# Performance work log

Measured on AMD Instinct MI355X. Metric: run time of the kernel, lower is better.

## Reference

```python
import jax, jax.numpy as jnp
import numpy as np

CAPS_N, DIMS_N, ROUNDS = 10, 16, 3
IN_CAPS_N, IN_DIMS_N = 1152, 8
BATCH = 256
EPS = 1e-7  # keras backend.epsilon()


def squash(x, axis=-1):
    sq = jnp.sum(x * x, axis=axis, keepdims=True)
    return (sq / (1.0 + sq)) * x / jnp.sqrt(sq + EPS)


def setup_inputs() -> dict:
    key = jax.random.key(0)
    k1, k2 = jax.random.split(key)
    inputs = jax.random.normal(k1, (BATCH, IN_CAPS_N, IN_DIMS_N), dtype=jnp.float32)
    # glorot-ish scale for the transform weights
    W = jax.random.normal(k2, (CAPS_N, IN_CAPS_N, DIMS_N, IN_DIMS_N), dtype=jnp.float32) * 0.05
    return {"inputs": inputs, "W": W}


def reference(inputs, W):
    # u_hat[b,j,i,d] = W[j,i] @ inputs[b,i]  (per-pair prediction vectors)
    u_hat = jnp.einsum('jide,bie->bjid', W, inputs)  # [B, caps_n, in_caps_n, dims_n]
    B = inputs.shape[0]
    cc = jnp.zeros((B, CAPS_N, IN_CAPS_N), dtype=u_hat.dtype)  # routing logits
    v = None
    for r in range(ROUNDS):
        c = jax.nn.softmax(cc, axis=1)                    # softmax over output capsules
        s = jnp.einsum('bji,bjid->bjd', c, u_hat)         # weighted sum over input caps
        v = squash(s, axis=-1)                            # [B, caps_n, dims_n]
        if r != ROUNDS - 1:
            cc = cc + jnp.einsum('bjid,bjd->bji', u_hat, v)  # agreement
    return v
```

## Files before the change

kernel.cpp:

```cpp
#include <hip/hip_runtime.h>

#define B_N 256
#define IC_N 1152
#define J_N 10
#define D_N 16

typedef __attribute__((ext_vector_type(8))) short short8;
typedef __attribute__((ext_vector_type(4))) float floatx4;

union u4s8 { uint4 u; short8 s; };

__device__ __forceinline__ float bf_lo(unsigned int u){
  union { unsigned int i; float f; } c; c.i = u << 16; return c.f;
}
__device__ __forceinline__ float bf_hi(unsigned int u){
  union { unsigned int i; float f; } c; c.i = u & 0xffff0000u; return c.f;
}
__device__ __forceinline__ unsigned int rne16(float f){
  union { float ff; unsigned int i; } c; c.ff = f;
  return (c.i + 0x7FFFu + ((c.i >> 16) & 1u)) >> 16;
}
__device__ __forceinline__ unsigned int pack_rne(float lo, float hi){
  return rne16(lo) | (rne16(hi) << 16);
}
__device__ __forceinline__ unsigned int pack_trunc(float lo, float hi){
  union { float f; unsigned int u; } a, b; a.f = lo; b.f = hi;
  return __builtin_amdgcn_perm(b.u, a.u, 0x07060302u);
}

__global__ __launch_bounds__(256) void caps_prep(
    const float* __restrict__ W, uint4* __restrict__ wsf,
    uint4* __restrict__ wcc2, float* __restrict__ vsum)
{
  const int tid = threadIdx.x;
  const int t0 = blockIdx.x * 256 + tid;
  if (t0 < B_N * J_N * D_N) vsum[t0] = 0.f;
  __shared__ unsigned int lw[1024];
  const int j = blockIdx.x / 72, itile = blockIdx.x % 72;
  const float4* Wt = (const float4*)(W + ((size_t)(j * IC_N + itile * 16) << 7));
  #pragma unroll
  for (int h = 0; h < 2; ++h) {
    const float4 f = Wt[h * 256 + tid];
    lw[(h * 256 + tid) * 2]     = pack_rne(f.x, f.y);
    lw[(h * 256 + tid) * 2 + 1] = pack_rne(f.z, f.w);
  }
  __syncthreads();
  {
    const int ktl = tid >> 6, ln = tid & 63;
    const int base = (ktl * 4 + (ln >> 4)) * 64 + (ln & 15) * 4;
    uint4 q;
    q.x = lw[base]; q.y = lw[base + 1]; q.z = lw[base + 2]; q.w = lw[base + 3];
    wsf[((size_t)j * 288 + itile * 4 + ktl) * 64 + ln] = q;
  }
  {
    const int e = tid >> 5, lane2 = tid & 31;
    const int il = lane2 & 15, dbase = (lane2 >> 4) * 8;
    unsigned short h[8];
    #pragma unroll
    for (int k = 0; k < 8; ++k) {
      const unsigned int u = lw[il * 64 + (dbase + k) * 4 + (e >> 1)];
      h[k] = (e & 1) ? (unsigned short)(u >> 16) : (unsigned short)(u & 0xffffu);
    }
    uint4 q;
    q.x = h[0] | ((unsigned int)h[1] << 16);
    q.y = h[2] | ((unsigned int)h[3] << 16);
    q.z = h[4] | ((unsigned int)h[5] << 16);
    q.w = h[6] | ((unsigned int)h[7] << 16);
    wcc2[(((size_t)j * 8 + e) * 72 + itile) * 32 + lane2] = q;
  }
}

__global__ __launch_bounds__(640, 5) void caps_pass(
    const float* __restrict__ x,
    const uint4* __restrict__ wsf, const uint4* __restrict__ wcc2,
    const uint4* __restrict__ vsbf, float* __restrict__ s_part, const int round)
{
  __shared__ float ccl[10 * 32 * 17];
  __shared__ unsigned int xt[32 * 17 * 4];

  const int tid  = threadIdx.x;
  const int wave = tid >> 6;
  const int lane = tid & 63;
  const int quad = lane >> 4;
  const int col  = lane & 15;

  const int bid = blockIdx.x;
  const int wid = (bid & 7) * 72 + (bid >> 3);
  const int bx  = wid & 15;
  const int by  = wid >> 4;
  const int b0  = bx << 4;
  const int i0  = by << 5;

  if (tid < 512) {
    const int b = tid >> 5, j4 = tid & 31;
    const int half = j4 & 1;
    #pragma unroll
    for (int ii = 0; ii < 2; ++ii) {
      const int i = ii * 16 + (j4 >> 1);
      const float4 v = ((const float4*)(x + ((size_t)((b0 + b) * IC_N + i0 + i) << 3)))[half];
      const int idx = ((i * 17 + b) << 2) + (half << 1);
      xt[idx]     = pack_rne(v.x, v.y);
      xt[idx + 1] = pack_rne(v.z, v.w);
    }
  }

  uint4 wf8[8];
  if (round == 0) {
    #pragma unroll
    for (int kt = 0; kt < 8; ++kt)
      wf8[kt] = wsf[((size_t)wave * 288 + (by << 3) + kt) * 64 + lane];
  }
  __syncthreads();
  const uint4* xtq = (const uint4*)xt;

  if (round > 0) {
    short8 av = {0,0,0,0,0,0,0,0};
    if (quad < 2)
      av = *(const short8*)&vsbf[((size_t)(b0 + col) * J_N + wave) * 2 + quad];
    #pragma unroll
    for (int c = 0; c < 2; ++c) {
      uint4 bvq[8];
      #pragma unroll
      for (int e = 0; e < 8; ++e) {
        uint4 q = {0u, 0u, 0u, 0u};
        if (lane < 32)
          q = wcc2[(((size_t)wave * 8 + e) * 72 + (by * 2 + c)) * 32 + lane];
        bvq[e] = q;
      }
      uint4 xr[4];
      #pragma unroll
      for (int r = 0; r < 4; ++r)
        xr[r] = xtq[(c * 16 + col) * 17 + quad * 4 + r];
      floatx4 cc4 = {0.f, 0.f, 0.f, 0.f};
      #pragma unroll
      for (int e = 0; e < 8; ++e) {
        u4s8 bv; bv.u = bvq[e];
        floatx4 tf = {0.f, 0.f, 0.f, 0.f};
        tf = __builtin_amdgcn_mfma_f32_16x16x32_bf16(av, bv.s, tf, 0, 0, 0);
        #pragma unroll
        for (int r = 0; r < 4; ++r) {
          const unsigned int u = ((const unsigned int*)&xr[r])[e >> 1];
          const float xe = (e & 1) ? bf_hi(u) : bf_lo(u);
          cc4[r] += tf[r] * xe;
        }
      }
      #pragma unroll
      for (int r = 0; r < 4; ++r)
        ccl[(wave * 32 + c * 16 + col) * 17 + quad * 4 + r] = cc4[r];
    }
    #pragma unroll
    for (int kt = 0; kt < 8; ++kt)
      wf8[kt] = wsf[((size_t)wave * 288 + (by << 3) + kt) * 64 + lane];
    __syncthreads();
    if (tid < 512) {
      const int i = tid >> 4, b = tid & 15;
      float cc[10];
      #pragma unroll
      for (int j = 0; j < 10; ++j) cc[j] = ccl[(j * 32 + i) * 17 + b];
      float m = cc[0];
      #pragma unroll
      for (int j = 1; j < 10; ++j) m = fmaxf(m, cc[j]);
      float den = 0.f;
      #pragma unroll
      for (int j = 0; j < 10; ++j) { cc[j] = __expf(cc[j] - m); den += cc[j]; }
      const float rd = __builtin_amdgcn_rcpf(den);
      #pragma unroll
      for (int j = 0; j < 10; ++j) ccl[(j * 32 + i) * 17 + b] = cc[j] * rd;
    }
    __syncthreads();
  }

  floatx4 acc0 = {0.f, 0.f, 0.f, 0.f};
  floatx4 acc1 = {0.f, 0.f, 0.f, 0.f};
  #pragma unroll
  for (int kt = 0; kt < 8; ++kt) {
    const int il = kt * 4 + quad;
    const uint4 xq = xtq[il * 17 + col];
    const float c = (round > 0) ? ccl[(wave * 32 + il) * 17 + col] : 0.1f;
    short8 af;
    unsigned int* aq = (unsigned int*)&af;
    aq[0] = pack_trunc(bf_lo(xq.x) * c, bf_hi(xq.x) * c);
    aq[1] = pack_trunc(bf_lo(xq.y) * c, bf_hi(xq.y) * c);
    aq[2] = pack_trunc(bf_lo(xq.z) * c, bf_hi(xq.z) * c);
    aq[3] = pack_trunc(bf_lo(xq.w) * c, bf_hi(xq.w) * c);
    u4s8 bw; bw.u = wf8[kt];
    if (kt & 1)
      acc1 = __builtin_amdgcn_mfma_f32_16x16x32_bf16(af, bw.s, acc1, 0, 0, 0);
    else
      acc0 = __builtin_amdgcn_mfma_f32_16x16x32_bf16(af, bw.s, acc0, 0, 0, 0);
  }
  const floatx4 acc = acc0 + acc1;
  float* sp = s_part + ((((size_t)bx * 10 + wave) * 16 + quad * 4) * 36
                        + by) * 16 + col;
  #pragma unroll
  for (int r = 0; r < 4; ++r) sp[(size_t)r * 36 * 16] = acc[r];
}

__global__ __launch_bounds__(256) void caps_squash(
    const float* __restrict__ s_part, float* __restrict__ vsum,
    unsigned int* __restrict__ vsbf_u, float* __restrict__ out, const int round)
{
  const int tid  = threadIdx.x;
  const int w    = tid >> 6;
  const int lane = tid & 63;
  const int bj   = blockIdx.x * 4 + w;
  const int b    = bj / 10, j = bj - b * 10;
  const int btile = b >> 4, brem = b & 15;
  const float* base = s_part + (((size_t)btile * 10 + j) * 16 + brem) * 576;
  float acc = 0.f;
  #pragma unroll
  for (int q = 0; q < 9; ++q) acc += base[q * 64 + lane];
  acc += __shfl_xor(acc, 16, 64);
  acc += __shfl_xor(acc, 32, 64);
  const float s = acc;
  float sq = s * s;
  sq += __shfl_xor(sq, 1, 16);
  sq += __shfl_xor(sq, 2, 16);
  sq += __shfl_xor(sq, 4, 16);
  sq += __shfl_xor(sq, 8, 16);
  const float coef = (sq / (1.f + sq)) * rsqrtf(sq + 1e-7f);
  const float v = coef * s;
  if (round < 2) {
    const float vprev = (lane < 16) ? vsum[bj * 16 + lane] : 0.f;
    const float vt = vprev + v;
    const float vtn = __shfl_down(vt, 1, 64);
    if (lane < 16) {
      vsum[bj * 16 + lane] = vt;
      if (!(lane & 1))
        vsbf_u[bj * 8 + (lane >> 1)] = pack_rne(vt, vtn);
    }
  } else if (lane < 16) {
    out[bj * 16 + lane] = v;
  }
}

extern "C" void kernel_launch(void* const* d_in, const int* in_sizes, int n_in,
                              void* d_out, int out_size, void* d_ws, size_t ws_size,
                              hipStream_t stream)
{
  const float* x_p = (const float*)d_in[0];
  const float* W_p = (const float*)d_in[1];

  uint4* wsf   = (uint4*)d_ws;
  uint4* wcc2  = wsf + 184320;
  float* s_prt = (float*)(wcc2 + 184320);
  float* vsum  = s_prt + 2949120;
  unsigned int* vsbf_u = (unsigned int*)(vsum + 40960);
  float* out_p = (float*)d_out;

  caps_prep<<<dim3(720), dim3(256), 0, stream>>>(W_p, wsf, wcc2, vsum);
  for (int r = 0; r < 3; ++r) {
    caps_pass<<<dim3(576), dim3(640), 0, stream>>>(
        x_p, wsf, wcc2, (const uint4*)vsbf_u, s_prt, r);
    caps_squash<<<dim3(640), dim3(256), 0, stream>>>(
        s_prt, vsum, vsbf_u, out_p, r);
  }
}
```

Baseline: 110.3 us.

## Pre-convert x to bf16 once in prep and hoist weight loads earlier

The prep kernel now converts the fp32 input x to packed bf16 once into workspace, so each of the three routing passes reads half the bytes and skips per-pass conversion. The pass kernel issues its weight-fragment loads at kernel start for all rounds, overlapping them with the x staging and routing work. The LDS operands are also preloaded into registers before the MFMA loop. Occupancy hint drops from 5 to 4 blocks per CU, trading occupancy for registers, and xbf is carved out of the s_part region of the workspace.

```diff
diff --git a/kernel.cpp b/kernel.cpp
--- a/kernel.cpp
+++ b/kernel.cpp
@@ -29,12 +29,17 @@
 }
 
 __global__ __launch_bounds__(256) void caps_prep(
-    const float* __restrict__ W, uint4* __restrict__ wsf,
-    uint4* __restrict__ wcc2, float* __restrict__ vsum)
+    const float* __restrict__ W, const float* __restrict__ x,
+    uint4* __restrict__ wsf, uint4* __restrict__ wcc2,
+    float* __restrict__ vsum, unsigned int* __restrict__ xbf)
 {
   const int tid = threadIdx.x;
   const int t0 = blockIdx.x * 256 + tid;
   if (t0 < B_N * J_N * D_N) vsum[t0] = 0.f;
+  for (int g = t0; g < B_N * IC_N * 4; g += 720 * 256) {
+    const float2 f = ((const float2*)x)[g];
+    xbf[g] = pack_rne(f.x, f.y);
+  }
   __shared__ unsigned int lw[1024];
   const int j = blockIdx.x / 72, itile = blockIdx.x % 72;
   const float4* Wt = (const float4*)(W + ((size_t)(j * IC_N + itile * 16) << 7));
@@ -70,8 +75,8 @@
   }
 }
 
-__global__ __launch_bounds__(640, 5) void caps_pass(
-    const float* __restrict__ x,
+__global__ __launch_bounds__(640, 4) void caps_pass(
+    const unsigned int* __restrict__ xbf,
     const uint4* __restrict__ wsf, const uint4* __restrict__ wcc2,
     const uint4* __restrict__ vsbf, float* __restrict__ s_part, const int round)
 {
@@ -91,24 +96,15 @@
   const int b0  = bx << 4;
   const int i0  = by << 5;
 
+  const uint4* wp = wsf + ((size_t)wave * 288 + (by << 3)) * 64 + lane;
+  uint4 wfv[8];
+  #pragma unroll
+  for (int kt = 0; kt < 8; ++kt) wfv[kt] = wp[(size_t)kt * 64];
+
   if (tid < 512) {
-    const int b = tid >> 5, j4 = tid & 31;
-    const int half = j4 & 1;
-    #pragma unroll
-    for (int ii = 0; ii < 2; ++ii) {
-      const int i = ii * 16 + (j4 >> 1);
-      const float4 v = ((const float4*)(x + ((size_t)((b0 + b) * IC_N + i0 + i) << 3)))[half];
-      const int idx = ((i * 17 + b) << 2) + (half << 1);
-      xt[idx]     = pack_rne(v.x, v.y);
-      xt[idx + 1] = pack_rne(v.z, v.w);
-    }
-  }
-
-  uint4 wf8[8];
-  if (round == 0) {
-    #pragma unroll
-    for (int kt = 0; kt < 8; ++kt)
-      wf8[kt] = wsf[((size_t)wave * 288 + (by << 3) + kt) * 64 + lane];
+    const int b = tid >> 5, i = tid & 31;
+    ((uint4*)xt)[i * 17 + b] =
+        ((const uint4*)xbf)[(size_t)(b0 + b) * IC_N + i0 + i];
   }
   __syncthreads();
   const uint4* xtq = (const uint4*)xt;
@@ -148,9 +144,6 @@
       for (int r = 0; r < 4; ++r)
         ccl[(wave * 32 + c * 16 + col) * 17 + quad * 4 + r] = cc4[r];
     }
-    #pragma unroll
-    for (int kt = 0; kt < 8; ++kt)
-      wf8[kt] = wsf[((size_t)wave * 288 + (by << 3) + kt) * 64 + lane];
     __syncthreads();
     if (tid < 512) {
       const int i = tid >> 4, b = tid & 15;
@@ -170,20 +163,27 @@
     __syncthreads();
   }
 
+  uint4 xv[8];
+  float cv[8];
+  #pragma unroll
+  for (int kt = 0; kt < 8; ++kt) {
+    const int il = kt * 4 + quad;
+    xv[kt] = xtq[il * 17 + col];
+    cv[kt] = (round > 0) ? ccl[(wave * 32 + il) * 17 + col] : 0.1f;
+  }
   floatx4 acc0 = {0.f, 0.f, 0.f, 0.f};
   floatx4 acc1 = {0.f, 0.f, 0.f, 0.f};
   #pragma unroll
   for (int kt = 0; kt < 8; ++kt) {
-    const int il = kt * 4 + quad;
-    const uint4 xq = xtq[il * 17 + col];
-    const float c = (round > 0) ? ccl[(wave * 32 + il) * 17 + col] : 0.1f;
+    const uint4 xq = xv[kt];
+    const float c = cv[kt];
     short8 af;
     unsigned int* aq = (unsigned int*)&af;
     aq[0] = pack_trunc(bf_lo(xq.x) * c, bf_hi(xq.x) * c);
     aq[1] = pack_trunc(bf_lo(xq.y) * c, bf_hi(xq.y) * c);
     aq[2] = pack_trunc(bf_lo(xq.z) * c, bf_hi(xq.z) * c);
     aq[3] = pack_trunc(bf_lo(xq.w) * c, bf_hi(xq.w) * c);
-    u4s8 bw; bw.u = wf8[kt];
+    u4s8 bw; bw.u = wfv[kt];
     if (kt & 1)
       acc1 = __builtin_amdgcn_mfma_f32_16x16x32_bf16(af, bw.s, acc1, 0, 0, 0);
     else
@@ -244,14 +244,15 @@
   uint4* wsf   = (uint4*)d_ws;
   uint4* wcc2  = wsf + 184320;
   float* s_prt = (float*)(wcc2 + 184320);
+  unsigned int* xbf = (unsigned int*)(s_prt + 1474560);
   float* vsum  = s_prt + 2949120;
   unsigned int* vsbf_u = (unsigned int*)(vsum + 40960);
   float* out_p = (float*)d_out;
 
-  caps_prep<<<dim3(720), dim3(256), 0, stream>>>(W_p, wsf, wcc2, vsum);
+  caps_prep<<<dim3(720), dim3(256), 0, stream>>>(W_p, x_p, wsf, wcc2, vsum, xbf);
   for (int r = 0; r < 3; ++r) {
     caps_pass<<<dim3(576), dim3(640), 0, stream>>>(
-        x_p, wsf, wcc2, (const uint4*)vsbf_u, s_prt, r);
+        xbf, wsf, wcc2, (const uint4*)vsbf_u, s_prt, r);
     caps_squash<<<dim3(640), dim3(256), 0, stream>>>(
         s_prt, vsum, vsbf_u, out_p, r);
   }
```

Measured after the change: 121.3 us. 9.9% more time.

## Process three input-capsule tiles per block with double-buffered prefetch

Applied to the files above, without the earlier changes.

Each caps_pass block now handles three consecutive 32-wide input-capsule tiles instead of one, so the grid shrinks from 576 to 192 blocks. Global loads of x, W fragments and agreement weights for the next tile are issued while the current tile computes, with the x tile double-buffered in shared memory. The goal is to hide global-load latency and amortise block setup. In exchange, register use rises (16 uint4 bvq plus prefetched x), launch bounds drop to 2 blocks per CU, and the smaller grid may leave compute units underused on a large GPU.

```diff
diff --git a/kernel.cpp b/kernel.cpp
--- a/kernel.cpp
+++ b/kernel.cpp
@@ -70,13 +70,13 @@
   }
 }
 
-__global__ __launch_bounds__(640, 5) void caps_pass(
+__global__ __launch_bounds__(640, 2) void caps_pass(
     const float* __restrict__ x,
     const uint4* __restrict__ wsf, const uint4* __restrict__ wcc2,
     const uint4* __restrict__ vsbf, float* __restrict__ s_part, const int round)
 {
   __shared__ float ccl[10 * 32 * 17];
-  __shared__ unsigned int xt[32 * 17 * 4];
+  __shared__ unsigned int xt[2][32 * 17 * 4];
 
   const int tid  = threadIdx.x;
   const int wave = tid >> 6;
@@ -85,115 +85,159 @@
   const int col  = lane & 15;
 
   const int bid = blockIdx.x;
-  const int wid = (bid & 7) * 72 + (bid >> 3);
-  const int bx  = wid & 15;
-  const int by  = wid >> 4;
+  const int w2  = (bid & 7) * 24 + (bid >> 3);
+  const int bx  = w2 & 15;
+  const int byg = w2 >> 4;
+  const int by0 = byg * 3;
   const int b0  = bx << 4;
-  const int i0  = by << 5;
-
+
+  const int sb = tid >> 5, sj4 = tid & 31;
+  const int shalf = sj4 & 1, si = sj4 >> 1;
+
+  float4 xA0, xA1, xB0, xB1;
   if (tid < 512) {
-    const int b = tid >> 5, j4 = tid & 31;
-    const int half = j4 & 1;
+    const float4* p = (const float4*)(x + ((size_t)((b0 + sb) * IC_N + (by0 << 5) + si) << 3));
+    xA0 = p[shalf]; xA1 = p[32 + shalf];
+  }
+  short8 av = {0,0,0,0,0,0,0,0};
+  if (round > 0 && quad < 2)
+    av = *(const short8*)&vsbf[((size_t)(b0 + col) * J_N + wave) * 2 + quad];
+  uint4 wf8[8];
+  #pragma unroll
+  for (int kt = 0; kt < 8; ++kt)
+    wf8[kt] = wsf[((size_t)wave * 288 + (by0 << 3) + kt) * 64 + lane];
+  uint4 bvq[16];
+  if (round > 0) {
     #pragma unroll
-    for (int ii = 0; ii < 2; ++ii) {
-      const int i = ii * 16 + (j4 >> 1);
-      const float4 v = ((const float4*)(x + ((size_t)((b0 + b) * IC_N + i0 + i) << 3)))[half];
-      const int idx = ((i * 17 + b) << 2) + (half << 1);
-      xt[idx]     = pack_rne(v.x, v.y);
-      xt[idx + 1] = pack_rne(v.z, v.w);
-    }
-  }
-
-  uint4 wf8[8];
-  if (round == 0) {
-    #pragma unroll
-    for (int kt = 0; kt < 8; ++kt)
-      wf8[kt] = wsf[((size_t)wave * 288 + (by << 3) + kt) * 64 + lane];
-  }
-  __syncthreads();
-  const uint4* xtq = (const uint4*)xt;
-
-  if (round > 0) {
-    short8 av = {0,0,0,0,0,0,0,0};
-    if (quad < 2)
-      av = *(const short8*)&vsbf[((size_t)(b0 + col) * J_N + wave) * 2 + quad];
-    #pragma unroll
-    for (int c = 0; c < 2; ++c) {
-      uint4 bvq[8];
+    for (int c = 0; c < 2; ++c)
       #pragma unroll
       for (int e = 0; e < 8; ++e) {
         uint4 q = {0u, 0u, 0u, 0u};
         if (lane < 32)
-          q = wcc2[(((size_t)wave * 8 + e) * 72 + (by * 2 + c)) * 32 + lane];
-        bvq[e] = q;
-      }
-      uint4 xr[4];
+          q = wcc2[(((size_t)wave * 8 + e) * 72 + (by0 * 2 + c)) * 32 + lane];
+        bvq[c * 8 + e] = q;
+      }
+  }
+  if (tid < 512) {
+    const int i0x = ((si * 17 + sb) << 2) + (shalf << 1);
+    xt[0][i0x]     = pack_rne(xA0.x, xA0.y);
+    xt[0][i0x + 1] = pack_rne(xA0.z, xA0.w);
+    const int i1x = (((16 + si) * 17 + sb) << 2) + (shalf << 1);
+    xt[0][i1x]     = pack_rne(xA1.x, xA1.y);
+    xt[0][i1x + 1] = pack_rne(xA1.z, xA1.w);
+    {
+      const float4* p = (const float4*)(x + ((size_t)((b0 + sb) * IC_N + ((by0 + 1) << 5) + si) << 3));
+      xB0 = p[shalf]; xB1 = p[32 + shalf];
+    }
+  }
+  __syncthreads();
+
+  #pragma unroll
+  for (int k = 0; k < 3; ++k) {
+    const int by  = by0 + k;
+    const int cur = k & 1;
+    const uint4* xtq = (const uint4*)xt[cur];
+
+    if (round > 0) {
       #pragma unroll
-      for (int r = 0; r < 4; ++r)
-        xr[r] = xtq[(c * 16 + col) * 17 + quad * 4 + r];
-      floatx4 cc4 = {0.f, 0.f, 0.f, 0.f};
+      for (int c = 0; c < 2; ++c) {
+        uint4 xr[4];
+        #pragma unroll
+        for (int r = 0; r < 4; ++r)
+          xr[r] = xtq[(c * 16 + col) * 17 + quad * 4 + r];
+        floatx4 cc4 = {0.f, 0.f, 0.f, 0.f};
+        #pragma unroll
+        for (int e = 0; e < 8; ++e) {
+          u4s8 bv; bv.u = bvq[c * 8 + e];
+          floatx4 tf = {0.f, 0.f, 0.f, 0.f};
+          tf = __builtin_amdgcn_mfma_f32_16x16x32_bf16(av, bv.s, tf, 0, 0, 0);
+          #pragma unroll
+          for (int r = 0; r < 4; ++r) {
+            const unsigned int u = ((const unsigned int*)&xr[r])[e >> 1];
+            const float xe = (e & 1) ? bf_hi(u) : bf_lo(u);
+            cc4[r] += tf[r] * xe;
+          }
+        }
+        #pragma unroll
+        for (int r = 0; r < 4; ++r)
+          ccl[(wave * 32 + c * 16 + col) * 17 + quad * 4 + r] = cc4[r];
+      }
+      if (k < 2) {
+        #pragma unroll
+        for (int c = 0; c < 2; ++c)
+          #pragma unroll
+          for (int e = 0; e < 8; ++e) {
+            uint4 q = {0u, 0u, 0u, 0u};
+            if (lane < 32)
+              q = wcc2[(((size_t)wave * 8 + e) * 72 + ((by + 1) * 2 + c)) * 32 + lane];
+            bvq[c * 8 + e] = q;
+          }
+      }
+      __syncthreads();
+      if (tid < 512) {
+        const int i = tid >> 4, b = tid & 15;
+        float cc[10];
+        #pragma unroll
+        for (int j = 0; j < 10; ++j) cc[j] = ccl[(j * 32 + i) * 17 + b];
+        float m = cc[0];
+        #pragma unroll
+        for (int j = 1; j < 10; ++j) m = fmaxf(m, cc[j]);
+        float den = 0.f;
+        #pragma unroll
+        for (int j = 0; j < 10; ++j) { cc[j] = __expf(cc[j] - m); den += cc[j]; }
+        const float rd = __builtin_amdgcn_rcpf(den);
+        #pragma unroll
+        for (int j = 0; j < 10; ++j) ccl[(j * 32 + i) * 17 + b] = cc[j] * rd;
+      }
+      __syncthreads();
+    }
+
+    floatx4 acc0 = {0.f, 0.f, 0.f, 0.f};
+    floatx4 acc1 = {0.f, 0.f, 0.f, 0.f};
+    #pragma unroll
+    for (int kt = 0; kt < 8; ++kt) {
+      const int il = kt * 4 + quad;
+      const uint4 xq = xtq[il * 17 + col];
+      const float c = (round > 0) ? ccl[(wave * 32 + il) * 17 + col] : 0.1f;
+      short8 af;
+      unsigned int* aq = (unsigned int*)&af;
+      aq[0] = pack_trunc(bf_lo(xq.x) * c, bf_hi(xq.x) * c);
+      aq[1] = pack_trunc(bf_lo(xq.y) * c, bf_hi(xq.y) * c);
+      aq[2] = pack_trunc(bf_lo(xq.z) * c, bf_hi(xq.z) * c);
+      aq[3] = pack_trunc(bf_lo(xq.w) * c, bf_hi(xq.w) * c);
+      u4s8 bw; bw.u = wf8[kt];
+      if (kt & 1)
+        acc1 = __builtin_amdgcn_mfma_f32_16x16x32_bf16(af, bw.s, acc1, 0, 0, 0);
+      else
+        acc0 = __builtin_amdgcn_mfma_f32_16x16x32_bf16(af, bw.s, acc0, 0, 0, 0);
+    }
+    const floatx4 acc = acc0 + acc1;
+    float* sp = s_part + ((((size_t)bx * 10 + wave) * 16 + quad * 4) * 36
+                          + by) * 16 + col;
+    #pragma unroll
+    for (int r = 0; r < 4; ++r) sp[(size_t)r * 36 * 16] = acc[r];
+
+    if (k < 2) {
       #pragma unroll
-      for (int e = 0; e < 8; ++e) {
-        u4s8 bv; bv.u = bvq[e];
-        floatx4 tf = {0.f, 0.f, 0.f, 0.f};
-        tf = __builtin_amdgcn_mfma_f32_16x16x32_bf16(av, bv.s, tf, 0, 0, 0);
-        #pragma unroll
-        for (int r = 0; r < 4; ++r) {
-          const unsigned int u = ((const unsigned int*)&xr[r])[e >> 1];
-          const float xe = (e & 1) ? bf_hi(u) : bf_lo(u);
-          cc4[r] += tf[r] * xe;
+      for (int kt = 0; kt < 8; ++kt)
+        wf8[kt] = wsf[((size_t)wave * 288 + ((by + 1) << 3) + kt) * 64 + lane];
+      if (tid < 512) {
+        const float4 v0 = (k == 0) ? xB0 : xA0;
+        const float4 v1 = (k == 0) ? xB1 : xA1;
+        const int i0x = ((si * 17 + sb) << 2) + (shalf << 1);
+        xt[cur ^ 1][i0x]     = pack_rne(v0.x, v0.y);
+        xt[cur ^ 1][i0x + 1] = pack_rne(v0.z, v0.w);
+        const int i1x = (((16 + si) * 17 + sb) << 2) + (shalf << 1);
+        xt[cur ^ 1][i1x]     = pack_rne(v1.x, v1.y);
+        xt[cur ^ 1][i1x + 1] = pack_rne(v1.z, v1.w);
+        if (k == 0) {
+          const float4* p = (const float4*)(x + ((size_t)((b0 + sb) * IC_N + ((by0 + 2) << 5) + si) << 3));
+          xA0 = p[shalf]; xA1 = p[32 + shalf];
         }
       }
-      #pragma unroll
-      for (int r = 0; r < 4; ++r)
-        ccl[(wave * 32 + c * 16 + col) * 17 + quad * 4 + r] = cc4[r];
-    }
-    #pragma unroll
-    for (int kt = 0; kt < 8; ++kt)
-      wf8[kt] = wsf[((size_t)wave * 288 + (by << 3) + kt) * 64 + lane];
-    __syncthreads();
-    if (tid < 512) {
-      const int i = tid >> 4, b = tid & 15;
-      float cc[10];
-      #pragma unroll
-      for (int j = 0; j < 10; ++j) cc[j] = ccl[(j * 32 + i) * 17 + b];
-      float m = cc[0];
-      #pragma unroll
-      for (int j = 1; j < 10; ++j) m = fmaxf(m, cc[j]);
-      float den = 0.f;
-      #pragma unroll
-      for (int j = 0; j < 10; ++j) { cc[j] = __expf(cc[j] - m); den += cc[j]; }
-      const float rd = __builtin_amdgcn_rcpf(den);
-      #pragma unroll
-      for (int j = 0; j < 10; ++j) ccl[(j * 32 + i) * 17 + b] = cc[j] * rd;
-    }
-    __syncthreads();
-  }
-
-  floatx4 acc0 = {0.f, 0.f, 0.f, 0.f};
-  floatx4 acc1 = {0.f, 0.f, 0.f, 0.f};
-  #pragma unroll
-  for (int kt = 0; kt < 8; ++kt) {
-    const int il = kt * 4 + quad;
-    const uint4 xq = xtq[il * 17 + col];
-    const float c = (round > 0) ? ccl[(wave * 32 + il) * 17 + col] : 0.1f;
-    short8 af;
-    unsigned int* aq = (unsigned int*)&af;
-    aq[0] = pack_trunc(bf_lo(xq.x) * c, bf_hi(xq.x) * c);
-    aq[1] = pack_trunc(bf_lo(xq.y) * c, bf_hi(xq.y) * c);
-    aq[2] = pack_trunc(bf_lo(xq.z) * c, bf_hi(xq.z) * c);
-    aq[3] = pack_trunc(bf_lo(xq.w) * c, bf_hi(xq.w) * c);
-    u4s8 bw; bw.u = wf8[kt];
-    if (kt & 1)
-      acc1 = __builtin_amdgcn_mfma_f32_16x16x32_bf16(af, bw.s, acc1, 0, 0, 0);
-    else
-      acc0 = __builtin_amdgcn_mfma_f32_16x16x32_bf16(af, bw.s, acc0, 0, 0, 0);
-  }
-  const floatx4 acc = acc0 + acc1;
-  float* sp = s_part + ((((size_t)bx * 10 + wave) * 16 + quad * 4) * 36
-                        + by) * 16 + col;
-  #pragma unroll
-  for (int r = 0; r < 4; ++r) sp[(size_t)r * 36 * 16] = acc[r];
+      __syncthreads();
+    }
+  }
 }
 
 __global__ __launch_bounds__(256) void caps_squash(
@@ -250,7 +294,7 @@
 
   caps_prep<<<dim3(720), dim3(256), 0, stream>>>(W_p, wsf, wcc2, vsum);
   for (int r = 0; r < 3; ++r) {
-    caps_pass<<<dim3(576), dim3(640), 0, stream>>>(
+    caps_pass<<<dim3(192), dim3(640), 0, stream>>>(
         x_p, wsf, wcc2, (const uint4*)vsbf_u, s_prt, r);
     caps_squash<<<dim3(640), dim3(256), 0, stream>>>(
         s_prt, vsum, vsbf_u, out_p, r);
```

Result: slower. 114.5 us (+3.8%).
